# Kernel tuning notes

Hardware: AMD Instinct MI355X
Metric: run time of the kernel (lower is better)

Reference implementation:

```python
import jax, jax.numpy as jnp
import numpy as np

CP_LEN = 256
FFT_SIZE = 1024
OFFSET = CP_LEN // 2                      # 128
PILOT_SPACING = 100
NSYMS = 824
TOTAL_SYMS = NSYMS + 1 + NSYMS // PILOT_SPACING   # 833
PAD_L = (FFT_SIZE - TOTAL_SYMS) // 2      # 95
PAD_R = FFT_SIZE - PAD_L - TOTAL_SYMS     # 96
PILOTS_IDX = np.arange(PAD_L, FFT_SIZE - PAD_R, PILOT_SPACING)  # 9 pilots

def _data_indices():
    # Statically unroll the original while-loop: gather all non-pilot data bins.
    idxs = []
    idx = 0
    jj = PAD_L + 1
    while idx < NSYMS:
        n = min(PILOT_SPACING - 1, NSYMS - idx)
        idxs.extend(range(jj, jj + n))
        idx += n
        jj += n + 1
    return np.asarray(idxs, dtype=np.int32)

DATA_IDX = _data_indices()  # [824]


def setup_inputs() -> dict:
    key = jax.random.key(0)
    # [batch, n_symbols, 2*(FFT_SIZE+CP_LEN)] interleaved I/Q floats
    in1 = jax.random.normal(key, (16, 1024, 2 * (FFT_SIZE + CP_LEN)), dtype=jnp.float32)
    return {"in1": in1}


def reference(in1):
    t = jnp.arange(FFT_SIZE, dtype=jnp.float32)
    # Deinterleave I/Q -> complex64
    iq = jax.lax.complex(in1[:, :, ::2], in1[:, :, 1::2])
    # FFT of the window starting at half the CP, then fftshift via roll
    spec = jnp.fft.fft(iq[:, :, OFFSET:OFFSET + FFT_SIZE], axis=2)
    result = jnp.roll(spec, FFT_SIZE // 2, axis=2)
    # Compensate timing-offset phase ramp
    result = result * jnp.exp(1j * OFFSET * t * (2.0 * np.pi / FFT_SIZE))
    # Estimate residual slope from pilot phase differences (wrapped to [-pi,pi])
    a = jnp.diff(jnp.angle(result[:, :, PILOTS_IDX]), axis=2)
    a = jnp.where(a > np.pi, a - 2.0 * np.pi, a)
    a = jnp.where(a < -np.pi, a + 2.0 * np.pi, a)
    mn = jnp.mean(a, axis=2)  # [B, S]
    result = result * jnp.exp(-1j * t * mn[:, :, None] / PILOT_SPACING)
    # Gather data (non-pilot) bins and interleave real/imag -> [B, S, 2*NSYMS]
    data = result[:, :, DATA_IDX]
    x = jnp.stack([data.real, data.imag], axis=-1).reshape(
        data.shape[0], data.shape[1], 2 * NSYMS)
    return x.astype(jnp.float32)
```

## Files before the change

kernel.cpp:

```cpp
#include <hip/hip_runtime.h>
#include <math.h>

#define NT      256
#define NSYMS   824
#define NPILOT  9

#define PADIDX(k) ((k) + ((k) >> 4))

#define C32_TWOPI_1024  6.1359233222901821136474609375e-3f

__device__ __forceinline__ float2 cmulf(float2 a, float2 b) {
    return make_float2(a.x * b.x - a.y * b.y, a.x * b.y + a.y * b.x);
}

template <int LM, int F>
__device__ __forceinline__ void dif_stage(float2* __restrict__ buf,
                                          const float2* __restrict__ W256,
                                          int i) {
    const int r = i & (LM - 1);
    const int base = ((i & ~(LM - 1)) << 2) | r;
    float2 a = buf[PADIDX(base)];
    float2 b = buf[PADIDX(base + LM)];
    float2 c = buf[PADIDX(base + 2 * LM)];
    float2 d = buf[PADIDX(base + 3 * LM)];
    float2 t0 = make_float2(a.x + c.x, a.y + c.y);
    float2 t1 = make_float2(a.x - c.x, a.y - c.y);
    float2 t2 = make_float2(b.x + d.x, b.y + d.y);
    float2 t3 = make_float2(b.x - d.x, b.y - d.y);
    float2 y0 = make_float2(t0.x + t2.x, t0.y + t2.y);
    float2 y1 = make_float2(t1.x + t3.y, t1.y - t3.x);
    float2 y2 = make_float2(t0.x - t2.x, t0.y - t2.y);
    float2 y3 = make_float2(t1.x - t3.y, t1.y + t3.x);
    const int e1 = F * r;
    const int e2 = 2 * F * r;
    const int e3 = 3 * F * r;
    float2 w1 = W256[PADIDX(e1)];
    float2 w2 = W256[PADIDX(e2 & 255)];
    if (e2 & 256) w2 = make_float2(w2.y, -w2.x);
    float2 w3 = W256[PADIDX(e3 & 255)];
    {
        const int q = e3 >> 8;
        if (q == 1)      w3 = make_float2(w3.y, -w3.x);
        else if (q == 2) w3 = make_float2(-w3.x, -w3.y);
    }
    buf[PADIDX(base)]          = y0;
    buf[PADIDX(base + LM)]     = cmulf(w1, y1);
    buf[PADIDX(base + 2 * LM)] = cmulf(w2, y2);
    buf[PADIDX(base + 3 * LM)] = cmulf(w3, y3);
}

__global__ void table_init(double2* __restrict__ Tg, float2* __restrict__ Wg) {
    const int t = threadIdx.x;
    double sn, cs;
    sincos((double)t * -6.1359231515425649189e-3, &sn, &cs);
    Tg[t] = make_double2(cs, sn);
    Wg[t] = make_float2((float)cs, (float)sn);
}

__global__ __launch_bounds__(NT, 8) void ofdm_kernel(const float* __restrict__ in,
                                                     float* __restrict__ out,
                                                     const double2* __restrict__ Tg,
                                                     const float2* __restrict__ Wg) {
    __shared__ double2 T256[256];
    __shared__ double2 u_s[NT];
    __shared__ float2  buf[1088];
    __shared__ float2  W256[272];
    __shared__ double  ang[NPILOT];

    const int row = blockIdx.x;
    const int tid = threadIdx.x;

    const float2* rin2 = (const float2*)(in + (size_t)row * 2560) + 128;
    float2 v0 = rin2[tid];
    float2 v1 = rin2[tid + 256];
    float2 v2 = rin2[tid + 512];
    float2 v3 = rin2[tid + 768];

    T256[tid] = Tg[tid];
    W256[PADIDX(tid)] = Wg[tid];

    double ux = ((double)v0.x - (double)v2.x) - ((double)v1.y - (double)v3.y);
    double uy = ((double)v0.y - (double)v2.y) + ((double)v1.x - (double)v3.x);

    buf[PADIDX(tid)]       = v0;
    buf[PADIDX(tid + 256)] = v1;
    buf[PADIDX(tid + 512)] = v2;
    buf[PADIDX(tid + 768)] = v3;
    u_s[tid] = make_double2(ux, uy);
    __syncthreads();

    if (tid < 16 * NPILOT) {
        const int p  = tid >> 4;
        const int g  = tid & 15;
        const int jj = 95 + 100 * p;
        const int K  = (jj + 512) & 1023;
        int idx = (K * g) & 1023;
        const int step = (K * 16) & 1023;
        double2 acc = make_double2(0.0, 0.0);
        #pragma unroll
        for (int m = 0; m < 16; m++) {
            double2 uu = u_s[g + 16 * m];
            double2 w  = T256[idx & 255];
            const int q = idx >> 8;
            double wx = w.x, wy = w.y;
            if (q & 1) { double t = wx; wx = wy; wy = -t; }
            if (q & 2) { wx = -wx; wy = -wy; }
            acc.x += wx * uu.x - wy * uu.y;
            acc.y += wx * uu.y + wy * uu.x;
            idx = (idx + step) & 1023;
        }
        #pragma unroll
        for (int off = 1; off < 16; off <<= 1) {
            acc.x += __shfl_xor(acc.x, off, 64);
            acc.y += __shfl_xor(acc.y, off, 64);
        }
        if (g == 0) {
            float th32 = (float)(128 * jj) * C32_TWOPI_1024;
            double sn, cs;
            sincos((double)th32, &sn, &cs);
            double csf = (double)(float)cs;
            double snf = (double)(float)sn;
            double re = acc.x * csf - acc.y * snf;
            double im = acc.x * snf + acc.y * csf;
            ang[p] = atan2(im, re);
        }
    }
    dif_stage<256, 1>(buf, W256, tid);
    __syncthreads();
    dif_stage<64, 4>(buf, W256, tid);
    __syncthreads();
    dif_stage<16, 16>(buf, W256, tid);
    __syncthreads();
    dif_stage<4, 64>(buf, W256, tid);
    __syncthreads();

    double mn;
    {
        double sum = 0.0;
        double prev = ang[0];
        #pragma unroll
        for (int k = 1; k < NPILOT; k++) {
            double cur = ang[k];
            double a = cur - prev;
            if (a > 3.14159265358979323846)       a -= 6.28318530717958647693;
            else if (a < -3.14159265358979323846) a += 6.28318530717958647693;
            sum += a;
            prev = cur;
        }
        mn = sum * 0.125;
    }

    {
        const int pb = PADIDX(4 * tid);
        float2 a = buf[pb];
        float2 b = buf[pb + 1];
        float2 c = buf[pb + 2];
        float2 d = buf[pb + 3];
        float2 t0 = make_float2(a.x + c.x, a.y + c.y);
        float2 t1 = make_float2(a.x - c.x, a.y - c.y);
        float2 t2 = make_float2(b.x + d.x, b.y + d.y);
        float2 t3 = make_float2(b.x - d.x, b.y - d.y);
        float2 y0 = make_float2(t0.x + t2.x, t0.y + t2.y);
        float2 y1 = make_float2(t1.x + t3.y, t1.y - t3.x);
        float2 y2 = make_float2(t0.x - t2.x, t0.y - t2.y);
        float2 y3 = make_float2(t1.x - t3.y, t1.y + t3.x);

        const int R = ((tid & 3) << 6) | (((tid >> 2) & 3) << 4) |
                      (((tid >> 4) & 3) << 2) | ((tid >> 6) & 3);

        float2* rout = (float2*)(out + (size_t)row * (2 * NSYMS));
        float2 ys[4] = { y2, y3, y0, y1 };
        #pragma unroll
        for (int k = 0; k < 4; k++) {
            const int jj = R + 256 * k;
            if (jj >= 96 && jj <= 927 && ((jj - 95) % 100) != 0) {
                const int dd = jj - 96 - (jj - 96) / 100;
                float2 z = ys[k];
                float th32 = (float)(128 * jj) * C32_TWOPI_1024;
                float ph = th32 - (float)(mn * 0.01 * (double)jj);
                float sn, cs;
                __sincosf(ph, &sn, &cs);
                rout[dd] = make_float2(z.x * cs - z.y * sn,
                                       z.x * sn + z.y * cs);
            }
        }
    }
}

extern "C" void kernel_launch(void* const* d_in, const int* in_sizes, int n_in,
                              void* d_out, int out_size, void* d_ws, size_t ws_size,
                              hipStream_t stream) {
    const float* in = (const float*)d_in[0];
    float* out = (float*)d_out;
    double2* Tg = (double2*)d_ws;
    float2*  Wg = (float2*)((char*)d_ws + 4096);
    table_init<<<dim3(1), dim3(256), 0, stream>>>(Tg, Wg);
    ofdm_kernel<<<dim3(16 * 1024), dim3(NT), 0, stream>>>(in, out, Tg, Wg);
}
```

Measured before the change: 281.5 us.

## Halve pilot DFT loop and parallelize pilot angle reduction with shuffles

The pilot DFT now folds two input samples per iteration using the 1024-point twiddle symmetry, halving the 16-step double-precision loop to 8 steps. The per-pilot atan2 and phase-rotation work moves out of the single g==0 lane of each 16-lane group into a separate stage run by one wave, placed between FFT stages. The serial loop in which every thread summed the 9 angle differences is replaced by a shuffle reduction that writes the slope once to shared memory. This aims to shorten the double-precision critical path, but adds a divergent branch inside the FFT stage and changes the floating-point summation order.

```diff
diff --git a/kernel.cpp b/kernel.cpp
--- a/kernel.cpp
+++ b/kernel.cpp
@@ -65,7 +65,8 @@
     __shared__ double2 u_s[NT];
     __shared__ float2  buf[1088];
     __shared__ float2  W256[272];
-    __shared__ double  ang[NPILOT];
+    __shared__ double2 pr2[NPILOT];
+    __shared__ double  mn_s;
 
     const int row = blockIdx.x;
     const int tid = threadIdx.x;
@@ -94,19 +95,25 @@
         const int g  = tid & 15;
         const int jj = 95 + 100 * p;
         const int K  = (jj + 512) & 1023;
+        const double sc = (p & 1) ? -0.70710678118654752440
+                                  :  0.70710678118654752440;
         int idx = (K * g) & 1023;
         const int step = (K * 16) & 1023;
         double2 acc = make_double2(0.0, 0.0);
         #pragma unroll
-        for (int m = 0; m < 16; m++) {
-            double2 uu = u_s[g + 16 * m];
+        for (int m = 0; m < 8; m++) {
+            const int s = g + 16 * m;
+            double2 u0 = u_s[s];
+            double2 u1 = u_s[s + 128];
+            double upx = u0.x + sc * (u1.x - u1.y);
+            double upy = u0.y + sc * (u1.x + u1.y);
             double2 w  = T256[idx & 255];
             const int q = idx >> 8;
             double wx = w.x, wy = w.y;
             if (q & 1) { double t = wx; wx = wy; wy = -t; }
             if (q & 2) { wx = -wx; wy = -wy; }
-            acc.x += wx * uu.x - wy * uu.y;
-            acc.y += wx * uu.y + wy * uu.x;
+            acc.x += wx * upx - wy * upy;
+            acc.y += wx * upy + wy * upx;
             idx = (idx + step) & 1023;
         }
         #pragma unroll
@@ -114,43 +121,44 @@
             acc.x += __shfl_xor(acc.x, off, 64);
             acc.y += __shfl_xor(acc.y, off, 64);
         }
-        if (g == 0) {
-            float th32 = (float)(128 * jj) * C32_TWOPI_1024;
-            double sn, cs;
-            sincos((double)th32, &sn, &cs);
-            double csf = (double)(float)cs;
-            double snf = (double)(float)sn;
-            double re = acc.x * csf - acc.y * snf;
-            double im = acc.x * snf + acc.y * csf;
-            ang[p] = atan2(im, re);
-        }
+        if (g == 0) pr2[p] = acc;
     }
     dif_stage<256, 1>(buf, W256, tid);
     __syncthreads();
+
     dif_stage<64, 4>(buf, W256, tid);
-    __syncthreads();
+    if (tid >= 192) {
+        const int p  = tid - 192;
+        const int pc = (p < 8) ? p : 8;
+        double2 acc = pr2[pc];
+        const int jj = 95 + 100 * pc;
+        float th32 = (float)(128 * jj) * C32_TWOPI_1024;
+        double sn, cs;
+        sincos((double)th32, &sn, &cs);
+        double csf = (double)(float)cs;
+        double snf = (double)(float)sn;
+        double re = acc.x * csf - acc.y * snf;
+        double im = acc.x * snf + acc.y * csf;
+        double a  = atan2(im, re);
+        double an = __shfl_down(a, 1, 64);
+        double d  = an - a;
+        if (d > 3.14159265358979323846)       d -= 6.28318530717958647693;
+        else if (d < -3.14159265358979323846) d += 6.28318530717958647693;
+        if (p >= 8) d = 0.0;
+        d += __shfl_xor(d, 1, 64);
+        d += __shfl_xor(d, 2, 64);
+        d += __shfl_xor(d, 4, 64);
+        if (p == 0) mn_s = d * 0.125;
+    }
+    __syncthreads();
+
     dif_stage<16, 16>(buf, W256, tid);
     __syncthreads();
     dif_stage<4, 64>(buf, W256, tid);
     __syncthreads();
 
-    double mn;
     {
-        double sum = 0.0;
-        double prev = ang[0];
-        #pragma unroll
-        for (int k = 1; k < NPILOT; k++) {
-            double cur = ang[k];
-            double a = cur - prev;
-            if (a > 3.14159265358979323846)       a -= 6.28318530717958647693;
-            else if (a < -3.14159265358979323846) a += 6.28318530717958647693;
-            sum += a;
-            prev = cur;
-        }
-        mn = sum * 0.125;
-    }
-
-    {
+        const double mn001 = mn_s * 0.01;
         const int pb = PADIDX(4 * tid);
         float2 a = buf[pb];
         float2 b = buf[pb + 1];
@@ -177,7 +185,7 @@
                 const int dd = jj - 96 - (jj - 96) / 100;
                 float2 z = ys[k];
                 float th32 = (float)(128 * jj) * C32_TWOPI_1024;
-                float ph = th32 - (float)(mn * 0.01 * (double)jj);
+                float ph = th32 - (float)(mn001 * (double)jj);
                 float sn, cs;
                 __sincosf(ph, &sn, &cs);
                 rout[dd] = make_float2(z.x * cs - z.y * sn,
```

After: 267.5 us. 1.05x faster.
